# Kernel tuning notes

Hardware: AMD Instinct MI355X
Metric: run time of the kernel (lower is better)

## Reference

```python
import jax, jax.numpy as jnp
import numpy as np
import math

B, N, D, H = 16, 1024, 1024, 8
HD = D // H
SCALE = 1.0 / math.sqrt(D // 8)
NEG = -1e30


def setup_inputs() -> dict:
    key = jax.random.key(0)
    ks = jax.random.split(key, 10)
    s = 0.02
    return {
        "x": jax.random.normal(ks[0], (B, N, D), dtype=jnp.float32),
        "x_mask": jax.random.randint(ks[1], (B, N), 0, 2, dtype=jnp.int32),
        "Wq": jax.random.normal(ks[2], (H, D, HD), dtype=jnp.float32) * s,
        "bq": jnp.zeros((H, HD), dtype=jnp.float32),
        "Wk": jax.random.normal(ks[3], (H, D, HD), dtype=jnp.float32) * s,
        "bk": jnp.zeros((H, HD), dtype=jnp.float32),
        "Wv": jax.random.normal(ks[4], (H, D, HD), dtype=jnp.float32) * s,
        "bv": jnp.zeros((H, HD), dtype=jnp.float32),
        "Wfc": jax.random.normal(ks[5], (D, D), dtype=jnp.float32) * s,
        "bfc": jnp.zeros((D,), dtype=jnp.float32),
    }


def reference(x, x_mask, Wq, bq, Wk, bk, Wv, bv, Wfc, bfc):
    # per-head projections, stacked: [B, H, N, HD]
    q = jnp.einsum("bnd,hde->bhne", x, Wq) + bq[None, :, None, :]
    k = jnp.einsum("bnd,hde->bhne", x, Wk) + bk[None, :, None, :]
    v = jnp.einsum("bnd,hde->bhne", x, Wv) + bv[None, :, None, :]
    # pairwise padding mask: mask & mask^T  ->  outer product for 0/1 values
    m = x_mask.astype(x.dtype)  # [B, N]
    mask = m[:, :, None] * m[:, None, :]  # [B, N, N]
    scores = jnp.einsum("bhne,bhme->bhnm", q, k) * SCALE  # [B, H, N, N]
    scores = scores * mask[:, None] + NEG * (1.0 - mask[:, None])
    attn = jax.nn.softmax(scores, axis=-1)
    o = jnp.einsum("bhnm,bhme->bhne", attn, v)  # [B, H, N, HD]
    # concat heads along feature dim (head order preserved)
    o = jnp.transpose(o, (0, 2, 1, 3)).reshape(B, N, D)
    out = o @ Wfc + bfc  # final fc; F.dropout result is discarded in source
    return out
```

## Files before the change

kernel.cpp:

```cpp
#include <hip/hip_runtime.h>
#include <hip/hip_bf16.h>
#include <math.h>

#define BN 1024
#define DD 1024
#define NB 16
#define NH 8
#define HDIM 128

typedef __attribute__((ext_vector_type(8))) short bf16x8;
typedef __attribute__((ext_vector_type(4))) float f32x4;
typedef __attribute__((ext_vector_type(4))) unsigned short ushort4v;

#define DEV __device__ __forceinline__

DEV unsigned short f2bf(float f) {
  unsigned u = __float_as_uint(f);
  u = (u + 0x7fffu + ((u >> 16) & 1u)) >> 16;
  return (unsigned short)u;
}

DEV f32x4 mfma16(bf16x8 a, bf16x8 b, f32x4 c) {
  return __builtin_amdgcn_mfma_f32_16x16x32_bf16(a, b, c, 0, 0, 0);
}

DEV void async16(const unsigned short* g, unsigned short* l) {
  __builtin_amdgcn_global_load_lds(
      (const __attribute__((address_space(1))) unsigned short*)g,
      (__attribute__((address_space(3))) unsigned short*)l, 16, 0, 0);
}

__global__ __launch_bounds__(256) void conv_x_kernel(const float* __restrict__ in,
                                                     unsigned short* __restrict__ out) {
  int i = blockIdx.x * 256 + threadIdx.x;
  const float4* p = (const float4*)in;
  float4 v = p[i];
  ushort4v o;
  o[0] = f2bf(v.x); o[1] = f2bf(v.y); o[2] = f2bf(v.z); o[3] = f2bf(v.w);
  *(ushort4v*)(out + (size_t)i * 4) = o;
}

__global__ __launch_bounds__(256) void transpose_qkv_kernel(const float* __restrict__ Wq,
                                                            const float* __restrict__ Wk,
                                                            const float* __restrict__ Wv,
                                                            unsigned short* __restrict__ outT) {
  __shared__ float tile[32][33];
  int z = blockIdx.z;
  int which = z >> 3, h = z & 7;
  const float* in = (which == 0 ? Wq : (which == 1 ? Wk : Wv)) + (size_t)h * DD * HDIM;
  int k0 = blockIdx.x * 32, e0 = blockIdx.y * 32;
  int tx = threadIdx.x, ty = threadIdx.y;
#pragma unroll
  for (int i = 0; i < 4; ++i)
    tile[ty + i * 8][tx] = in[(size_t)(k0 + ty + i * 8) * HDIM + e0 + tx];
  __syncthreads();
  int rowbase = which * 1024 + h * 128 + e0;
#pragma unroll
  for (int i = 0; i < 4; ++i)
    outT[(size_t)(rowbase + ty + i * 8) * DD + k0 + tx] = f2bf(tile[tx][ty + i * 8]);
}

__global__ __launch_bounds__(256) void transpose_fc_kernel(const float* __restrict__ W,
                                                           unsigned short* __restrict__ outT) {
  __shared__ float tile[32][33];
  int d0 = blockIdx.x * 32, c0 = blockIdx.y * 32;
  int tx = threadIdx.x, ty = threadIdx.y;
#pragma unroll
  for (int i = 0; i < 4; ++i)
    tile[ty + i * 8][tx] = W[(size_t)(d0 + ty + i * 8) * DD + c0 + tx];
  __syncthreads();
#pragma unroll
  for (int i = 0; i < 4; ++i)
    outT[(size_t)(c0 + ty + i * 8) * DD + d0 + tx] = f2bf(tile[tx][ty + i * 8]);
}

template <int MODE>
__global__ __launch_bounds__(256, 3) void gemm128_kernel(
    const unsigned short* __restrict__ A, const unsigned short* __restrict__ Bt,
    const float* __restrict__ bias0, const float* __restrict__ bias1,
    const float* __restrict__ bias2, unsigned short* __restrict__ out0,
    unsigned short* __restrict__ out1, unsigned short* __restrict__ out2,
    float* __restrict__ outf) {
  __shared__ unsigned short as[128 * 32];
  __shared__ unsigned short bs[128 * 32];
  const int tid = threadIdx.x;
  const int wave = tid >> 6, lane = tid & 63, quad = lane >> 4, l15 = lane & 15;
  const int wr = wave >> 1, wc = wave & 1;
  const int m0 = (blockIdx.x & 127) << 7, n0 = (blockIdx.x >> 7) << 7;
  f32x4 acc[4][4] = {};

  const int srow = wave * 32 + (lane >> 2);
  const int scol = (lane & 3) * 8;
  const unsigned short* ag = A + (size_t)(m0 + srow) * 1024 + scol;
  const unsigned short* bg = Bt + (size_t)(n0 + srow) * 1024 + scol;
  unsigned short* as_w = as + wave * 1024;
  unsigned short* bs_w = bs + wave * 1024;

  for (int kb = 0; kb < 1024; kb += 32) {
    async16(ag + kb, as_w);
    async16(ag + kb + 16 * 1024, as_w + 512);
    async16(bg + kb, bs_w);
    async16(bg + kb + 16 * 1024, bs_w + 512);
    __syncthreads();
    bf16x8 af[4], bfr[4];
#pragma unroll
    for (int mt = 0; mt < 4; ++mt)
      af[mt] = *(const bf16x8*)(as + (wr * 64 + mt * 16 + l15) * 32 + quad * 8);
#pragma unroll
    for (int nt = 0; nt < 4; ++nt)
      bfr[nt] = *(const bf16x8*)(bs + (wc * 64 + nt * 16 + l15) * 32 + quad * 8);
#pragma unroll
    for (int mt = 0; mt < 4; ++mt)
#pragma unroll
      for (int nt = 0; nt < 4; ++nt)
        acc[mt][nt] = mfma16(af[mt], bfr[nt], acc[mt][nt]);
    __syncthreads();
  }

  if constexpr (MODE == 0) {
    const int seg = n0 >> 10;
#pragma unroll
    for (int mt = 0; mt < 4; ++mt) {
      int mb = m0 + wr * 64 + mt * 16 + quad * 4;
      int bb = mb >> 10, nn = mb & 1023;
#pragma unroll
      for (int nt = 0; nt < 4; ++nt) {
        int c = n0 + wc * 64 + nt * 16 + l15;
        int cc = c & 1023;
        int h = cc >> 7, e = cc & 127;
        if (seg == 2) {
          float bias = bias2[cc];
          ushort4v pv;
#pragma unroll
          for (int r = 0; r < 4; ++r) pv[r] = f2bf(acc[mt][nt][r] + bias);
          *(ushort4v*)(out2 + ((size_t)(bb * NH + h) * HDIM + e) * BN + nn) = pv;
        } else {
          const float* bp = (seg == 0) ? bias0 : bias1;
          unsigned short* op = (seg == 0) ? out0 : out1;
          float bias = bp[cc];
#pragma unroll
          for (int r = 0; r < 4; ++r)
            op[(((size_t)bb * NH + h) * BN + (nn + r)) * HDIM + e] =
                f2bf(acc[mt][nt][r] + bias);
        }
      }
    }
  } else {
#pragma unroll
    for (int mt = 0; mt < 4; ++mt) {
      int mb = m0 + wr * 64 + mt * 16 + quad * 4;
#pragma unroll
      for (int nt = 0; nt < 4; ++nt) {
        int c = n0 + wc * 64 + nt * 16 + l15;
        float bias = bias0[c];
#pragma unroll
        for (int r = 0; r < 4; ++r)
          outf[(size_t)(mb + r) * DD + c] = acc[mt][nt][r] + bias;
      }
    }
  }
}

__global__ __launch_bounds__(256, 2) void flash_attn_kernel(
    const unsigned short* __restrict__ Q, const unsigned short* __restrict__ Kk,
    const unsigned short* __restrict__ Vt, const int* __restrict__ xmask,
    unsigned short* __restrict__ O) {
  __shared__ unsigned short k_s[64 * 136];
  __shared__ unsigned short v_s[128 * 72];
  __shared__ unsigned short p_s[4][32 * 72];

  const float CL2E = 0.08838834764831845f * 1.44269504088896f;

  const int tid = threadIdx.x;
  const int w = tid >> 6, lane = tid & 63, quad = lane >> 4, l15 = lane & 15;
  const int lin = blockIdx.x;
  const int bh = lin & 127, qb = lin >> 7;
  const int b = bh >> 3, h = bh & 7;
  const int q0 = qb * 128;
  const unsigned short* qp = Q + ((size_t)bh * BN + q0) * HDIM;
  const unsigned short* kp = Kk + (size_t)bh * BN * HDIM;
  const unsigned short* vp = Vt + (size_t)bh * HDIM * BN;
  const int* xm_b = xmask + b * BN;

  bf16x8 qf[2][4];
#pragma unroll
  for (int mt = 0; mt < 2; ++mt)
#pragma unroll
    for (int ks = 0; ks < 4; ++ks)
      qf[mt][ks] = *(const bf16x8*)(qp + (w * 32 + mt * 16 + l15) * HDIM + ks * 32 + quad * 8);

  int rowm[2][4];
#pragma unroll
  for (int mt = 0; mt < 2; ++mt)
#pragma unroll
    for (int r = 0; r < 4; ++r)
      rowm[mt][r] = xm_b[q0 + w * 32 + mt * 16 + quad * 4 + r];

  float l_lane[2][4] = {};
  f32x4 o_acc[2][8] = {};

  for (int kb = 0; kb < BN; kb += 64) {
#pragma unroll
    for (int it = 0; it < 4; ++it) {
      int c = it * 256 + tid;
      int row = c >> 4, off = (c & 15) * 8;
      *(bf16x8*)(k_s + row * 136 + off) = *(const bf16x8*)(kp + (size_t)(kb + row) * HDIM + off);
    }
#pragma unroll
    for (int it = 0; it < 4; ++it) {
      int c = it * 256 + tid;
      int row = c >> 3, off = (c & 7) * 8;
      *(bf16x8*)(v_s + row * 72 + off) = *(const bf16x8*)(vp + (size_t)row * BN + kb + off);
    }
    int cm[4];
#pragma unroll
    for (int nt = 0; nt < 4; ++nt) cm[nt] = xm_b[kb + nt * 16 + l15];
    __syncthreads();

    f32x4 s[2][4] = {};
#pragma unroll
    for (int ks = 0; ks < 4; ++ks) {
      bf16x8 bfr[4];
#pragma unroll
      for (int nt = 0; nt < 4; ++nt)
        bfr[nt] = *(const bf16x8*)(k_s + (nt * 16 + l15) * 136 + ks * 32 + quad * 8);
#pragma unroll
      for (int mt = 0; mt < 2; ++mt)
#pragma unroll
        for (int nt = 0; nt < 4; ++nt)
          s[mt][nt] = mfma16(qf[mt][ks], bfr[nt], s[mt][nt]);
    }

#pragma unroll
    for (int mt = 0; mt < 2; ++mt)
#pragma unroll
      for (int nt = 0; nt < 4; ++nt)
#pragma unroll
        for (int r = 0; r < 4; ++r) {
          float xs = s[mt][nt][r] * CL2E;
          float t = cm[nt] ? xs : -60.0f;
          float e2 = rowm[mt][r] ? t : 0.0f;
          float p = __builtin_amdgcn_exp2f(e2);
          l_lane[mt][r] += p;
          p_s[w][(mt * 16 + quad * 4 + r) * 72 + nt * 16 + l15] = f2bf(p);
        }

#pragma unroll
    for (int ks2 = 0; ks2 < 2; ++ks2) {
      bf16x8 pa[2];
#pragma unroll
      for (int mt = 0; mt < 2; ++mt)
        pa[mt] = *(const bf16x8*)(p_s[w] + (mt * 16 + l15) * 72 + ks2 * 32 + quad * 8);
#pragma unroll
      for (int et = 0; et < 8; ++et) {
        bf16x8 bv = *(const bf16x8*)(v_s + (et * 16 + l15) * 72 + ks2 * 32 + quad * 8);
#pragma unroll
        for (int mt = 0; mt < 2; ++mt)
          o_acc[mt][et] = mfma16(pa[mt], bv, o_acc[mt][et]);
      }
    }
    __syncthreads();
  }

#pragma unroll
  for (int mt = 0; mt < 2; ++mt)
#pragma unroll
    for (int r = 0; r < 4; ++r) {
      float l = l_lane[mt][r];
#pragma unroll
      for (int off = 1; off < 16; off <<= 1) l += __shfl_xor(l, off, 64);
      float inv = 1.0f / l;
      int row = q0 + w * 32 + mt * 16 + quad * 4 + r;
#pragma unroll
      for (int et = 0; et < 8; ++et) {
        int col = h * HDIM + et * 16 + l15;
        O[((size_t)b * BN + row) * DD + col] = f2bf(o_acc[mt][et][r] * inv);
      }
    }
}

extern "C" void kernel_launch(void* const* d_in, const int* in_sizes, int n_in,
                              void* d_out, int out_size, void* d_ws, size_t ws_size,
                              hipStream_t stream) {
  const float* x = (const float*)d_in[0];
  const int* xmask = (const int*)d_in[1];
  const float* Wq = (const float*)d_in[2];
  const float* bq = (const float*)d_in[3];
  const float* Wk = (const float*)d_in[4];
  const float* bk = (const float*)d_in[5];
  const float* Wv = (const float*)d_in[6];
  const float* bv = (const float*)d_in[7];
  const float* Wfc = (const float*)d_in[8];
  const float* bfc = (const float*)d_in[9];
  float* out = (float*)d_out;

  char* ws = (char*)d_ws;
  unsigned short* x_bf  = (unsigned short*)(ws);
  unsigned short* wqkvT = (unsigned short*)(ws + 33554432);
  unsigned short* wfcT  = (unsigned short*)(ws + 39845888);
  unsigned short* q_bf  = (unsigned short*)(ws + 41943040);
  unsigned short* k_bf  = (unsigned short*)(ws + 75497472);
  unsigned short* vT_bf = (unsigned short*)(ws + 109051904);
  unsigned short* o_bf  = (unsigned short*)(ws + 142606336);

  conv_x_kernel<<<dim3(16384), dim3(256), 0, stream>>>(x, x_bf);
  transpose_qkv_kernel<<<dim3(32, 4, 24), dim3(32, 8), 0, stream>>>(Wq, Wk, Wv, wqkvT);
  transpose_fc_kernel<<<dim3(32, 32), dim3(32, 8), 0, stream>>>(Wfc, wfcT);

  gemm128_kernel<0><<<dim3(3072), dim3(256), 0, stream>>>(
      x_bf, wqkvT, bq, bk, bv, q_bf, k_bf, vT_bf, nullptr);

  flash_attn_kernel<<<dim3(1024), dim3(256), 0, stream>>>(q_bf, k_bf, vT_bf, xmask, o_bf);

  gemm128_kernel<1><<<dim3(1024), dim3(256), 0, stream>>>(
      o_bf, wfcT, bfc, nullptr, nullptr, nullptr, nullptr, nullptr, out);
}
```

Baseline: 418.6 us.

## Swizzle LDS layouts with async global-to-LDS loads and fuse prep kernels

Merges the x conversion and the two weight-transpose kernels into one prep launch. The GEMM now stages K-tiles of 64 instead of 32, using an XOR-style rotated chunk layout in LDS to avoid bank conflicts, which halves the number of barriers per K. The attention kernel replaces register-staged K/V copies into padded LDS with direct global_load_lds async loads into unpadded, rotation-swizzled tiles, cutting VGPR traffic and LDS footprint. Correctness depends on the swizzle read and write indices matching exactly.

```diff
diff --git a/kernel.cpp b/kernel.cpp
--- a/kernel.cpp
+++ b/kernel.cpp
@@ -30,48 +30,47 @@
       (__attribute__((address_space(3))) unsigned short*)l, 16, 0, 0);
 }
 
-__global__ __launch_bounds__(256) void conv_x_kernel(const float* __restrict__ in,
-                                                     unsigned short* __restrict__ out) {
-  int i = blockIdx.x * 256 + threadIdx.x;
-  const float4* p = (const float4*)in;
-  float4 v = p[i];
-  ushort4v o;
-  o[0] = f2bf(v.x); o[1] = f2bf(v.y); o[2] = f2bf(v.z); o[3] = f2bf(v.w);
-  *(ushort4v*)(out + (size_t)i * 4) = o;
-}
-
-__global__ __launch_bounds__(256) void transpose_qkv_kernel(const float* __restrict__ Wq,
-                                                            const float* __restrict__ Wk,
-                                                            const float* __restrict__ Wv,
-                                                            unsigned short* __restrict__ outT) {
+__global__ __launch_bounds__(256) void prep_kernel(
+    const float* __restrict__ x, const float* __restrict__ Wq,
+    const float* __restrict__ Wk, const float* __restrict__ Wv,
+    const float* __restrict__ Wfc, unsigned short* __restrict__ x_bf,
+    unsigned short* __restrict__ wqkvT, unsigned short* __restrict__ wfcT) {
   __shared__ float tile[32][33];
-  int z = blockIdx.z;
-  int which = z >> 3, h = z & 7;
-  const float* in = (which == 0 ? Wq : (which == 1 ? Wk : Wv)) + (size_t)h * DD * HDIM;
-  int k0 = blockIdx.x * 32, e0 = blockIdx.y * 32;
-  int tx = threadIdx.x, ty = threadIdx.y;
-#pragma unroll
-  for (int i = 0; i < 4; ++i)
-    tile[ty + i * 8][tx] = in[(size_t)(k0 + ty + i * 8) * HDIM + e0 + tx];
-  __syncthreads();
-  int rowbase = which * 1024 + h * 128 + e0;
-#pragma unroll
-  for (int i = 0; i < 4; ++i)
-    outT[(size_t)(rowbase + ty + i * 8) * DD + k0 + tx] = f2bf(tile[tx][ty + i * 8]);
-}
-
-__global__ __launch_bounds__(256) void transpose_fc_kernel(const float* __restrict__ W,
-                                                           unsigned short* __restrict__ outT) {
-  __shared__ float tile[32][33];
-  int d0 = blockIdx.x * 32, c0 = blockIdx.y * 32;
-  int tx = threadIdx.x, ty = threadIdx.y;
-#pragma unroll
-  for (int i = 0; i < 4; ++i)
-    tile[ty + i * 8][tx] = W[(size_t)(d0 + ty + i * 8) * DD + c0 + tx];
-  __syncthreads();
-#pragma unroll
-  for (int i = 0; i < 4; ++i)
-    outT[(size_t)(c0 + ty + i * 8) * DD + d0 + tx] = f2bf(tile[tx][ty + i * 8]);
+  const int bx = blockIdx.x, tid = threadIdx.x;
+  if (bx < 16384) {
+    int i = bx * 256 + tid;
+    const float4* p = (const float4*)x;
+    float4 v = p[i];
+    ushort4v o;
+    o[0] = f2bf(v.x); o[1] = f2bf(v.y); o[2] = f2bf(v.z); o[3] = f2bf(v.w);
+    *(ushort4v*)(x_bf + (size_t)i * 4) = o;
+    return;
+  }
+  const int tx = tid & 31, ty = tid >> 5;
+  if (bx < 19456) {
+    int idx = bx - 16384;
+    int k0 = (idx & 31) * 32, e0 = ((idx >> 5) & 3) * 32, z = idx >> 7;
+    int which = z >> 3, h = z & 7;
+    const float* in = (which == 0 ? Wq : (which == 1 ? Wk : Wv)) + (size_t)h * DD * HDIM;
+#pragma unroll
+    for (int i = 0; i < 4; ++i)
+      tile[ty + i * 8][tx] = in[(size_t)(k0 + ty + i * 8) * HDIM + e0 + tx];
+    __syncthreads();
+    int rowbase = which * 1024 + h * 128 + e0;
+#pragma unroll
+    for (int i = 0; i < 4; ++i)
+      wqkvT[(size_t)(rowbase + ty + i * 8) * DD + k0 + tx] = f2bf(tile[tx][ty + i * 8]);
+  } else {
+    int idx = bx - 19456;
+    int d0 = (idx & 31) * 32, c0 = (idx >> 5) * 32;
+#pragma unroll
+    for (int i = 0; i < 4; ++i)
+      tile[ty + i * 8][tx] = Wfc[(size_t)(d0 + ty + i * 8) * DD + c0 + tx];
+    __syncthreads();
+#pragma unroll
+    for (int i = 0; i < 4; ++i)
+      wfcT[(size_t)(c0 + ty + i * 8) * DD + d0 + tx] = f2bf(tile[tx][ty + i * 8]);
+  }
 }
 
 template <int MODE>
@@ -81,39 +80,44 @@
     const float* __restrict__ bias2, unsigned short* __restrict__ out0,
     unsigned short* __restrict__ out1, unsigned short* __restrict__ out2,
     float* __restrict__ outf) {
-  __shared__ unsigned short as[128 * 32];
-  __shared__ unsigned short bs[128 * 32];
+  __shared__ unsigned short as[128 * 64];
+  __shared__ unsigned short bs[128 * 64];
   const int tid = threadIdx.x;
   const int wave = tid >> 6, lane = tid & 63, quad = lane >> 4, l15 = lane & 15;
   const int wr = wave >> 1, wc = wave & 1;
   const int m0 = (blockIdx.x & 127) << 7, n0 = (blockIdx.x >> 7) << 7;
   f32x4 acc[4][4] = {};
 
-  const int srow = wave * 32 + (lane >> 2);
-  const int scol = (lane & 3) * 8;
-  const unsigned short* ag = A + (size_t)(m0 + srow) * 1024 + scol;
-  const unsigned short* bg = Bt + (size_t)(n0 + srow) * 1024 + scol;
-  unsigned short* as_w = as + wave * 1024;
-  unsigned short* bs_w = bs + wave * 1024;
-
-  for (int kb = 0; kb < 1024; kb += 32) {
-    async16(ag + kb, as_w);
-    async16(ag + kb + 16 * 1024, as_w + 512);
-    async16(bg + kb, bs_w);
-    async16(bg + kb + 16 * 1024, bs_w + 512);
-    __syncthreads();
-    bf16x8 af[4], bfr[4];
-#pragma unroll
-    for (int mt = 0; mt < 4; ++mt)
-      af[mt] = *(const bf16x8*)(as + (wr * 64 + mt * 16 + l15) * 32 + quad * 8);
-#pragma unroll
-    for (int nt = 0; nt < 4; ++nt)
-      bfr[nt] = *(const bf16x8*)(bs + (wc * 64 + nt * 16 + l15) * 32 + quad * 8);
-#pragma unroll
-    for (int mt = 0; mt < 4; ++mt)
+  const int srow = wave * 32 + (lane >> 3);
+  const int gch = ((lane & 7) - (lane >> 3)) & 7;
+  const unsigned short* ag = A + (size_t)(m0 + srow) * 1024 + gch * 8;
+  const unsigned short* bg = Bt + (size_t)(n0 + srow) * 1024 + gch * 8;
+  unsigned short* as_w = as + wave * 32 * 64;
+  unsigned short* bs_w = bs + wave * 32 * 64;
+
+  for (int kb = 0; kb < 1024; kb += 64) {
+#pragma unroll
+    for (int i = 0; i < 4; ++i) {
+      async16(ag + kb + i * 8 * 1024, as_w + i * 512);
+      async16(bg + kb + i * 8 * 1024, bs_w + i * 512);
+    }
+    __syncthreads();
+#pragma unroll
+    for (int ks = 0; ks < 2; ++ks) {
+      const int sl = ((quad + ks * 4 + l15) & 7) * 8;
+      bf16x8 af[4], bfr[4];
+#pragma unroll
+      for (int mt = 0; mt < 4; ++mt)
+        af[mt] = *(const bf16x8*)(as + (wr * 64 + mt * 16 + l15) * 64 + sl);
 #pragma unroll
       for (int nt = 0; nt < 4; ++nt)
-        acc[mt][nt] = mfma16(af[mt], bfr[nt], acc[mt][nt]);
+        bfr[nt] = *(const bf16x8*)(bs + (wc * 64 + nt * 16 + l15) * 64 + sl);
+#pragma unroll
+      for (int mt = 0; mt < 4; ++mt)
+#pragma unroll
+        for (int nt = 0; nt < 4; ++nt)
+          acc[mt][nt] = mfma16(af[mt], bfr[nt], acc[mt][nt]);
+    }
     __syncthreads();
   }
 
@@ -165,8 +169,8 @@
     const unsigned short* __restrict__ Q, const unsigned short* __restrict__ Kk,
     const unsigned short* __restrict__ Vt, const int* __restrict__ xmask,
     unsigned short* __restrict__ O) {
-  __shared__ unsigned short k_s[64 * 136];
-  __shared__ unsigned short v_s[128 * 72];
+  __shared__ unsigned short k_s[64 * 128];
+  __shared__ unsigned short v_s[128 * 64];
   __shared__ unsigned short p_s[4][32 * 72];
 
   const float CL2E = 0.08838834764831845f * 1.44269504088896f;
@@ -196,21 +200,25 @@
     for (int r = 0; r < 4; ++r)
       rowm[mt][r] = xm_b[q0 + w * 32 + mt * 16 + quad * 4 + r];
 
+  const int krow = lane >> 4;
+  const int vrow = lane >> 3;
+  const int vch = ((lane & 7) - vrow) & 7;
+
   float l_lane[2][4] = {};
   f32x4 o_acc[2][8] = {};
 
   for (int kb = 0; kb < BN; kb += 64) {
 #pragma unroll
-    for (int it = 0; it < 4; ++it) {
-      int c = it * 256 + tid;
-      int row = c >> 4, off = (c & 15) * 8;
-      *(bf16x8*)(k_s + row * 136 + off) = *(const bf16x8*)(kp + (size_t)(kb + row) * HDIM + off);
-    }
-#pragma unroll
-    for (int it = 0; it < 4; ++it) {
-      int c = it * 256 + tid;
-      int row = c >> 3, off = (c & 7) * 8;
-      *(bf16x8*)(v_s + row * 72 + off) = *(const bf16x8*)(vp + (size_t)row * BN + kb + off);
+    for (int i = 0; i < 4; ++i) {
+      int rmod = i * 4 + krow;
+      int g = ((lane & 15) - rmod) & 15;
+      async16(kp + (size_t)(kb + w * 16 + rmod) * HDIM + g * 8,
+              k_s + (w * 16 + i * 4) * 128);
+    }
+#pragma unroll
+    for (int i = 0; i < 4; ++i) {
+      int e = w * 32 + i * 8 + vrow;
+      async16(vp + (size_t)e * BN + kb + vch * 8, v_s + (w * 32 + i * 8) * 64);
     }
     int cm[4];
 #pragma unroll
@@ -220,10 +228,11 @@
     f32x4 s[2][4] = {};
 #pragma unroll
     for (int ks = 0; ks < 4; ++ks) {
+      const int sl = ((ks * 4 + quad + l15) & 15) * 8;
       bf16x8 bfr[4];
 #pragma unroll
       for (int nt = 0; nt < 4; ++nt)
-        bfr[nt] = *(const bf16x8*)(k_s + (nt * 16 + l15) * 136 + ks * 32 + quad * 8);
+        bfr[nt] = *(const bf16x8*)(k_s + (nt * 16 + l15) * 128 + sl);
 #pragma unroll
       for (int mt = 0; mt < 2; ++mt)
 #pragma unroll
@@ -247,13 +256,14 @@
 
 #pragma unroll
     for (int ks2 = 0; ks2 < 2; ++ks2) {
+      const int sl = ((ks2 * 4 + quad + l15) & 7) * 8;
       bf16x8 pa[2];
 #pragma unroll
       for (int mt = 0; mt < 2; ++mt)
         pa[mt] = *(const bf16x8*)(p_s[w] + (mt * 16 + l15) * 72 + ks2 * 32 + quad * 8);
 #pragma unroll
       for (int et = 0; et < 8; ++et) {
-        bf16x8 bv = *(const bf16x8*)(v_s + (et * 16 + l15) * 72 + ks2 * 32 + quad * 8);
+        bf16x8 bv = *(const bf16x8*)(v_s + (et * 16 + l15) * 64 + sl);
 #pragma unroll
         for (int mt = 0; mt < 2; ++mt)
           o_acc[mt][et] = mfma16(pa[mt], bv, o_acc[mt][et]);
@@ -303,9 +313,7 @@
   unsigned short* vT_bf = (unsigned short*)(ws + 109051904);
   unsigned short* o_bf  = (unsigned short*)(ws + 142606336);
 
-  conv_x_kernel<<<dim3(16384), dim3(256), 0, stream>>>(x, x_bf);
-  transpose_qkv_kernel<<<dim3(32, 4, 24), dim3(32, 8), 0, stream>>>(Wq, Wk, Wv, wqkvT);
-  transpose_fc_kernel<<<dim3(32, 32), dim3(32, 8), 0, stream>>>(Wfc, wfcT);
+  prep_kernel<<<dim3(20480), dim3(256), 0, stream>>>(x, Wq, Wk, Wv, Wfc, x_bf, wqkvT, wfcT);
 
   gemm128_kernel<0><<<dim3(3072), dim3(256), 0, stream>>>(
       x_bf, wqkvT, bq, bk, bv, q_bf, k_bf, vT_bf, nullptr);
```

Measured after the change: 409.5 us. 2.2% less time.
